# Kernel optimization log

Hardware: AMD Instinct MI355X
Metric: run time of the kernel (lower is better)

Reference implementation:

```python
import jax, jax.numpy as jnp
import numpy as np

N, E, G, F = 100000, 3200000, 256, 15
NEG_SLOPE = 0.2


def _lin(k, fi, fo):
    s = 1.0 / np.sqrt(fi)
    return jax.random.uniform(k, (fi, fo), jnp.float32, -s, s)


def _vec(k, n, fi):
    s = 1.0 / np.sqrt(fi)
    return jax.random.uniform(k, (n,), jnp.float32, -s, s)


def setup_inputs() -> dict:
    key = jax.random.key(0)
    ks = jax.random.split(key, 40)
    inp = {}
    inp["x"] = jax.random.normal(ks[0], (N, F), jnp.float32)
    inp["edge_index"] = jax.random.randint(ks[1], (2, E), 0, N, dtype=jnp.int32)
    inp["batch"] = jnp.sort(jax.random.randint(ks[2], (N,), 0, G, dtype=jnp.int32))
    inp["xA"] = jax.random.normal(ks[3], (G, 300), jnp.float32)
    i = 4
    for l in (1, 2, 3):
        inp[f"cW{l}"] = _lin(ks[i], F, F); i += 1
        inp[f"cas{l}"] = _vec(ks[i], F, F); i += 1
        inp[f"cad{l}"] = _vec(ks[i], F, F); i += 1
        inp[f"cb{l}"] = jnp.zeros((F,), jnp.float32)
        inp[f"fW{l}"] = _lin(ks[i], F, F); i += 1
        inp[f"fb{l}"] = _vec(ks[i], F, F); i += 1
    inp["m1W"] = _lin(ks[i], 90, 90); i += 1
    inp["m1b"] = _vec(ks[i], 90, 90); i += 1
    inp["aW1"] = _lin(ks[i], 300, 300); i += 1
    inp["ab1"] = _vec(ks[i], 300, 300); i += 1
    inp["aW2"] = _lin(ks[i], 300, 300); i += 1
    inp["ab2"] = _vec(ks[i], 300, 300); i += 1
    inp["aW3"] = _lin(ks[i], 300, 300); i += 1
    inp["ab3"] = _vec(ks[i], 300, 300); i += 1
    inp["aW4"] = _lin(ks[i], 300, 45); i += 1
    inp["ab4"] = _vec(ks[i], 45, 300); i += 1
    inp["m2W"] = _lin(ks[i], 90, 1); i += 1
    inp["m2b"] = _vec(ks[i], 1, 90); i += 1
    return inp


def _gat(x, src, dst, W, a_s, a_d, b):
    """PyG GATConv (heads=1, add_self_loops handled by caller via src/dst)."""
    h = x @ W                                        # [N, F]
    e = jax.nn.leaky_relu((h @ a_s)[src] + (h @ a_d)[dst], NEG_SLOPE)  # [E+N]
    mx = jax.ops.segment_max(e, dst, num_segments=N)
    ex = jnp.exp(e - mx[dst])
    den = jax.ops.segment_sum(ex, dst, num_segments=N)
    alpha = ex / (den[dst] + 1e-16)                   # segment softmax over dst
    out = jax.ops.segment_sum(h[src] * alpha[:, None], dst, num_segments=N)
    return out + b


def reference(x, edge_index, batch, xA,
              cW1, cas1, cad1, cb1, fW1, fb1,
              cW2, cas2, cad2, cb2, fW2, fb2,
              cW3, cas3, cad3, cb3, fW3, fb3,
              m1W, m1b, aW1, ab1, aW2, ab2, aW3, ab3, aW4, ab4,
              m2W, m2b):
    loop = jnp.arange(N, dtype=edge_index.dtype)      # self loops
    src = jnp.concatenate([edge_index[0], loop])
    dst = jnp.concatenate([edge_index[1], loop])

    h = _gat(x, src, dst, cW1, cas1, cad1, cb1)
    h = jax.nn.relu(h @ fW1 + fb1)
    h = _gat(h, src, dst, cW2, cas2, cad2, cb2)
    h = jax.nn.relu(h @ fW2 + fb2)
    h = _gat(h, src, dst, cW3, cas3, cad3, cb3)
    h = h @ fW3 + fb3

    s = jax.ops.segment_sum(h, batch, num_segments=G)
    mx = jax.ops.segment_max(h, batch, num_segments=G)
    cnt = jax.ops.segment_sum(jnp.ones((N, 1), h.dtype), batch, num_segments=G)
    mean = s / jnp.maximum(cnt, 1.0)
    pooled = jnp.concatenate([s, mx, mean], axis=1)   # [G, 45]

    a = jax.nn.relu(xA @ aW1 + ab1)
    a = jax.nn.relu(a @ aW2 + ab2)
    a = jax.nn.sigmoid(a @ aW3 + ab3)
    xann = a @ aW4 + ab4                              # [G, 45]

    z = jnp.concatenate([pooled, xann], axis=1)       # [G, 90]
    z = jax.nn.relu(z @ m1W + m1b)
    z = z @ m2W + m2b
    return jax.nn.sigmoid(z)
```

## Files before the change

kernel.cpp:

```cpp
#include <hip/hip_runtime.h>
#include <hip/hip_bf16.h>
#include <math.h>

#define FDIM 15
#define FPAD 16
#define NEG_SLOPE 0.2f
#define BSH 8
#define BWID 256
#define HB_GRID 256
#define HB_BLK 1024

typedef _Float16 half_t;

__device__ __forceinline__ float leaky(float e) {
  return fmaxf(NEG_SLOPE * e, e);
}

__global__ void k_zero(int* __restrict__ p, int n) {
  int i = blockIdx.x * blockDim.x + threadIdx.x;
  if (i < n) p[i] = 0;
}

__global__ void k_bhist(const int* __restrict__ dstI, int* __restrict__ bcnt,
                        int n_tot, int n_real, int NB) {
  __shared__ int hist[512];
  int tid = threadIdx.x;
  for (int i = tid; i < NB; i += blockDim.x) hist[i] = 0;
  __syncthreads();
  int stride = gridDim.x * blockDim.x;
  for (int i = blockIdx.x * blockDim.x + tid; i < n_tot; i += stride) {
    int d = (i < n_real) ? dstI[i] : (i - n_real);
    atomicAdd(&hist[d >> BSH], 1);
  }
  __syncthreads();
  for (int i = tid; i < NB; i += blockDim.x)
    if (hist[i]) atomicAdd(&bcnt[i], hist[i]);
}

__global__ void k_bscan(const int* __restrict__ bcnt, int* __restrict__ boff,
                        int* __restrict__ bcur, int* __restrict__ rowptr,
                        int NB, int N, int total) {
  __shared__ int s[512];
  int tid = threadIdx.x;
  int v = (tid < NB) ? bcnt[tid] : 0;
  s[tid] = v;
  __syncthreads();
  for (int off = 1; off < 512; off <<= 1) {
    int add = (tid >= off) ? s[tid - off] : 0;
    __syncthreads();
    s[tid] += add;
    __syncthreads();
  }
  if (tid < NB) { int e = s[tid] - v; boff[tid] = e; bcur[tid] = e; }
  if (tid == NB - 1) boff[NB] = s[tid];
  if (tid == 0) rowptr[N] = total;
}

__global__ void k_bpart(const int* __restrict__ srcI, const int* __restrict__ dstI,
                        int* __restrict__ bcur, int* __restrict__ bbuf,
                        int n_tot, int n_real, int NB) {
  __shared__ int hist[512];
  __shared__ int base[512];
  int tid = threadIdx.x;
  for (int i = tid; i < NB; i += blockDim.x) hist[i] = 0;
  __syncthreads();
  int stride = gridDim.x * blockDim.x;
  int g0 = blockIdx.x * blockDim.x + tid;
  for (int i = g0; i < n_tot; i += stride) {
    int d = (i < n_real) ? dstI[i] : (i - n_real);
    atomicAdd(&hist[d >> BSH], 1);
  }
  __syncthreads();
  for (int i = tid; i < NB; i += blockDim.x)
    base[i] = hist[i] ? atomicAdd(&bcur[i], hist[i]) : 0;
  __syncthreads();
  for (int i = tid; i < NB; i += blockDim.x) hist[i] = 0;
  __syncthreads();
  for (int i = g0; i < n_tot; i += stride) {
    int s, d;
    if (i < n_real) { s = srcI[i]; d = dstI[i]; }
    else { s = d = i - n_real; }
    int b = d >> BSH;
    int p = base[b] + atomicAdd(&hist[b], 1);
    bbuf[p] = (s << BSH) | (d & (BWID - 1));
  }
}

__global__ void k_bbuild(const int* __restrict__ boff, const int* __restrict__ bbuf,
                         int* __restrict__ rowptr, int* __restrict__ csr, int N) {
  __shared__ int hist[BWID];
  __shared__ int sc[BWID];
  int b = blockIdx.x;
  int tid = threadIdx.x;
  int base_dst = b << BSH;
  int nd = min(BWID, N - base_dst);
  int s0 = boff[b], s1 = boff[b + 1];
  if (tid < BWID) hist[tid] = 0;
  __syncthreads();
  for (int j = s0 + tid; j < s1; j += 512)
    atomicAdd(&hist[bbuf[j] & (BWID - 1)], 1);
  __syncthreads();
  int v = 0;
  if (tid < BWID) { v = hist[tid]; sc[tid] = v; }
  __syncthreads();
  for (int off = 1; off < BWID; off <<= 1) {
    int add = 0;
    if (tid < BWID && tid >= off) add = sc[tid - off];
    __syncthreads();
    if (tid < BWID) sc[tid] += add;
    __syncthreads();
  }
  if (tid < nd) rowptr[base_dst + tid] = s0 + sc[tid] - v;
  __syncthreads();
  if (tid < BWID) hist[tid] = sc[tid] - v;
  __syncthreads();
  for (int j = s0 + tid; j < s1; j += 512) {
    int e = bbuf[j];
    int dl = e & (BWID - 1);
    int p = s0 + atomicAdd(&hist[dl], 1);
    csr[p] = (e >> BSH) << 5;
  }
}

__global__ void k_transform(const float* __restrict__ in, int ld_in,
                            const float* __restrict__ W,
                            const float* __restrict__ a_s,
                            const float* __restrict__ a_d,
                            half_t* __restrict__ hp,
                            float* __restrict__ ad_,
                            int n_nodes) {
  __shared__ float Ws[FDIM * FDIM];
  __shared__ float asv[FDIM], adv[FDIM];
  int tid = threadIdx.x;
  if (tid < FDIM * FDIM) Ws[tid] = W[tid];
  if (tid < FDIM) { asv[tid] = a_s[tid]; adv[tid] = a_d[tid]; }
  __syncthreads();
  int n = blockIdx.x * blockDim.x + tid;
  if (n >= n_nodes) return;
  float xin[FDIM];
#pragma unroll
  for (int j = 0; j < FDIM; ++j) xin[j] = in[n * ld_in + j];
  float sa = 0.f, da = 0.f;
  half_t hrow[FPAD];
#pragma unroll
  for (int o = 0; o < FDIM; ++o) {
    float acc = 0.f;
#pragma unroll
    for (int k = 0; k < FDIM; ++k) acc += xin[k] * Ws[k * FDIM + o];
    hrow[o] = (half_t)acc;
    sa += acc * asv[o];
    da += acc * adv[o];
  }
  hrow[FDIM] = (half_t)sa;
  ad_[n] = da;
  float4 w0, w1;
  __builtin_memcpy(&w0, &hrow[0], 16);
  __builtin_memcpy(&w1, &hrow[8], 16);
  float4* dst = (float4*)(hp + (size_t)n * FPAD);
  dst[0] = w0;
  dst[1] = w1;
}

__global__ void k_gat(const int* __restrict__ rowptr, const int* __restrict__ csrB,
                      const half_t* __restrict__ hp, const float* __restrict__ ad_,
                      const float* __restrict__ cb, const float* __restrict__ fW,
                      const float* __restrict__ fb,
                      const float* __restrict__ nW, const float* __restrict__ nas,
                      const float* __restrict__ nad,
                      half_t* __restrict__ hp2, float* __restrict__ ad2,
                      float* __restrict__ fout,
                      int n_nodes, int do_relu, int fuse) {
  __shared__ float Ws[FDIM * FDIM];
  __shared__ float W2s[FDIM * FDIM];
  __shared__ float cbv[FDIM], fbv[FDIM], as2v[FDIM], ad2v[FDIM];
  __shared__ float aggT[16][16];
  __shared__ float outT[16][16];
  int tid = threadIdx.x;
  if (tid < FDIM * FDIM) Ws[tid] = fW[tid];
  if (tid < FDIM) { cbv[tid] = cb[tid]; fbv[tid] = fb[tid]; }
  if (fuse) {
    if (tid < FDIM * FDIM) W2s[tid] = nW[tid];
    if (tid < FDIM) { as2v[tid] = nas[tid]; ad2v[tid] = nad[tid]; }
  }
  __syncthreads();
  int dl = tid >> 4;
  int f  = tid & 15;
  int d  = blockIdx.x * 16 + dl;
  float val = 0.f;
  if (d < n_nodes) {
    int rs = rowptr[d], re = rowptr[d + 1];
    float adv = ad_[d];
    const char* hb = (const char*)hp;
    int fo = f << 1;
    float den0 = 0.f, acc0 = 0.f, den1 = 0.f, acc1 = 0.f;
    int j = rs;
    for (; j + 7 < re; j += 8) {
      int o0 = csrB[j],     o1 = csrB[j + 1], o2 = csrB[j + 2], o3 = csrB[j + 3];
      int o4 = csrB[j + 4], o5 = csrB[j + 5], o6 = csrB[j + 6], o7 = csrB[j + 7];
      float hv0 = (float)*(const half_t*)(hb + o0 + fo);
      float hv1 = (float)*(const half_t*)(hb + o1 + fo);
      float hv2 = (float)*(const half_t*)(hb + o2 + fo);
      float hv3 = (float)*(const half_t*)(hb + o3 + fo);
      float hv4 = (float)*(const half_t*)(hb + o4 + fo);
      float hv5 = (float)*(const half_t*)(hb + o5 + fo);
      float hv6 = (float)*(const half_t*)(hb + o6 + fo);
      float hv7 = (float)*(const half_t*)(hb + o7 + fo);
      float w0 = __expf(leaky(__shfl(hv0, 15, 16) + adv));
      float w1 = __expf(leaky(__shfl(hv1, 15, 16) + adv));
      float w2 = __expf(leaky(__shfl(hv2, 15, 16) + adv));
      float w3 = __expf(leaky(__shfl(hv3, 15, 16) + adv));
      float w4 = __expf(leaky(__shfl(hv4, 15, 16) + adv));
      float w5 = __expf(leaky(__shfl(hv5, 15, 16) + adv));
      float w6 = __expf(leaky(__shfl(hv6, 15, 16) + adv));
      float w7 = __expf(leaky(__shfl(hv7, 15, 16) + adv));
      den0 += w0; acc0 += hv0 * w0;
      den1 += w1; acc1 += hv1 * w1;
      den0 += w2; acc0 += hv2 * w2;
      den1 += w3; acc1 += hv3 * w3;
      den0 += w4; acc0 += hv4 * w4;
      den1 += w5; acc1 += hv5 * w5;
      den0 += w6; acc0 += hv6 * w6;
      den1 += w7; acc1 += hv7 * w7;
    }
    for (; j < re; ++j) {
      int o0 = csrB[j];
      float hv0 = (float)*(const half_t*)(hb + o0 + fo);
      float w0 = __expf(leaky(__shfl(hv0, 15, 16) + adv));
      den0 += w0; acc0 += hv0 * w0;
    }
    val = (acc0 + acc1) / (den0 + den1 + 1e-16f);
  }
  aggT[dl][f] = (f < FDIM) ? (val + cbv[f]) : 0.f;
  __syncthreads();
  int o = f;
  float ffn = 0.f;
  if (o < FDIM) {
    ffn = fbv[o];
#pragma unroll
    for (int k = 0; k < FDIM; ++k) ffn += aggT[dl][k] * Ws[k * FDIM + o];
    if (do_relu) ffn = fmaxf(ffn, 0.f);
  }
  if (!fuse) {
    if (d < n_nodes) fout[d * FPAD + o] = (o < FDIM) ? ffn : 0.f;
    return;
  }
  outT[dl][o] = ffn;
  __syncthreads();
  if (d < n_nodes) {
    float h2 = 0.f;
    if (o < FDIM) {
#pragma unroll
      for (int k = 0; k < FDIM; ++k) h2 += outT[dl][k] * W2s[k * FDIM + o];
    }
    float pa = (o < FDIM) ? h2 * as2v[o] : 0.f;
    float pd = (o < FDIM) ? h2 * ad2v[o] : 0.f;
#pragma unroll
    for (int k = 8; k; k >>= 1) {
      pa += __shfl_xor(pa, k, 16);
      pd += __shfl_xor(pd, k, 16);
    }
    hp2[(size_t)d * FPAD + o] = (half_t)((o < FDIM) ? h2 : pa);
    if (o == 0) ad2[d] = pd;
  }
}

__device__ __forceinline__ int lowerb(const int* __restrict__ a, int n, int key) {
  int lo = 0, hi = n;
  while (lo < hi) { int mid = (lo + hi) >> 1; if (a[mid] < key) lo = mid + 1; else hi = mid; }
  return lo;
}

__global__ void k_pool(const float* __restrict__ fout, const int* __restrict__ batch,
                       float* __restrict__ pooled, int n_nodes) {
  __shared__ float ss[256], sm[256];
  int g = blockIdx.x;
  int tid = threadIdx.x;
  int s = lowerb(batch, n_nodes, g);
  int e = lowerb(batch, n_nodes, g + 1);
  int f = tid & 15;
  float sum = 0.f, mx = -INFINITY;
  for (int n = s + (tid >> 4); n < e; n += 16) {
    float v = fout[n * FPAD + f];
    sum += v;
    mx = fmaxf(mx, v);
  }
  ss[tid] = sum; sm[tid] = mx;
  __syncthreads();
  for (int step = 128; step >= 16; step >>= 1) {
    if (tid < step) { ss[tid] += ss[tid + step]; sm[tid] = fmaxf(sm[tid], sm[tid + step]); }
    __syncthreads();
  }
  if (tid < FDIM) {
    float cnt = (float)(e - s);
    float sv = ss[tid];
    pooled[g * 45 + tid] = sv;
    pooled[g * 45 + 15 + tid] = sm[tid];
    pooled[g * 45 + 30 + tid] = sv / fmaxf(cnt, 1.f);
  }
}

__global__ void k_ann(const float* __restrict__ xA,
                      const float* __restrict__ aW1, const float* __restrict__ ab1,
                      const float* __restrict__ aW2, const float* __restrict__ ab2,
                      const float* __restrict__ aW3, const float* __restrict__ ab3,
                      const float* __restrict__ aW4, const float* __restrict__ ab4,
                      const float* __restrict__ m1W, const float* __restrict__ m1b,
                      const float* __restrict__ m2W, const float* __restrict__ m2b,
                      const float* __restrict__ pooled,
                      float* __restrict__ out) {
  __shared__ float za[304], zb[304];
  int g = blockIdx.x;
  int t = threadIdx.x;
  for (int k = t; k < 300; k += 320) za[k] = xA[g * 300 + k];
  __syncthreads();
  if (t < 300) {
    float acc = ab1[t];
#pragma unroll 10
    for (int k = 0; k < 300; ++k) acc += za[k] * aW1[k * 300 + t];
    zb[t] = fmaxf(acc, 0.f);
  }
  __syncthreads();
  if (t < 300) {
    float acc = ab2[t];
#pragma unroll 10
    for (int k = 0; k < 300; ++k) acc += zb[k] * aW2[k * 300 + t];
    za[t] = fmaxf(acc, 0.f);
  }
  __syncthreads();
  if (t < 300) {
    float acc = ab3[t];
#pragma unroll 10
    for (int k = 0; k < 300; ++k) acc += za[k] * aW3[k * 300 + t];
    zb[t] = 1.f / (1.f + expf(-acc));
  }
  __syncthreads();
  if (t < 45) {
    float acc = ab4[t];
#pragma unroll 10
    for (int k = 0; k < 300; ++k) acc += zb[k] * aW4[k * 45 + t];
    za[45 + t] = acc;
  } else if (t < 90) {
    za[t - 45] = pooled[g * 45 + (t - 45)];
  }
  __syncthreads();
  if (t < 90) {
    float acc = m1b[t];
#pragma unroll 10
    for (int k = 0; k < 90; ++k) acc += za[k] * m1W[k * 90 + t];
    zb[t] = fmaxf(acc, 0.f);
  }
  __syncthreads();
  if (t == 0) {
    float acc = m2b[0];
#pragma unroll 10
    for (int k = 0; k < 90; ++k) acc += zb[k] * m2W[k];
    out[g] = 1.f / (1.f + expf(-acc));
  }
}

extern "C" void kernel_launch(void* const* d_in, const int* in_sizes, int n_in,
                              void* d_out, int out_size, void* d_ws, size_t ws_size,
                              hipStream_t stream) {
  const float* x   = (const float*)d_in[0];
  const int* ei    = (const int*)d_in[1];
  const int* batch = (const int*)d_in[2];
  const float* xA  = (const float*)d_in[3];

  const int N = in_sizes[0] / FDIM;
  const int E = in_sizes[1] / 2;
  const int G = in_sizes[3] / 300;
  const int ET = E + N;
  const int NB = (N + BWID - 1) >> BSH;

  const int* srcI = ei;
  const int* dstI = ei + E;

  float* ws = (float*)d_ws;
  size_t layerW = (size_t)34 * N;
  size_t uSize = layerW > (size_t)ET ? layerW : (size_t)ET;
  size_t off = 0;
  int*    bbuf = (int*)(ws + off);
  half_t* hpA  = (half_t*)(ws + off);
  half_t* hpB  = (half_t*)(ws + off + (size_t)8 * N);
  float*  adA  = ws + off + (size_t)16 * N;
  float*  adB  = ws + off + (size_t)17 * N;
  float*  fout = ws + off + (size_t)18 * N;
  off += uSize;
  int*   rowptr = (int*)(ws + off); off += N + 1;
  int*   csr    = (int*)(ws + off); off += (size_t)ET;
  int*   bcnt   = (int*)(ws + off); off += 516;
  int*   boff   = (int*)(ws + off); off += 516;
  int*   bcur   = (int*)(ws + off); off += 516;
  float* pooled = ws + off; off += (size_t)G * 45;

  const int B = 256;
  const int gN = (N + B - 1) / B;

  k_zero<<<(NB + B - 1) / B, B, 0, stream>>>(bcnt, NB);
  k_bhist<<<HB_GRID, HB_BLK, 0, stream>>>(dstI, bcnt, ET, E, NB);
  k_bscan<<<1, 512, 0, stream>>>(bcnt, boff, bcur, rowptr, NB, N, ET);
  k_bpart<<<HB_GRID, HB_BLK, 0, stream>>>(srcI, dstI, bcur, bbuf, ET, E, NB);
  k_bbuild<<<NB, 512, 0, stream>>>(boff, bbuf, rowptr, csr, N);

  const float* cW1  = (const float*)d_in[4];
  const float* cas1 = (const float*)d_in[5];
  const float* cad1 = (const float*)d_in[6];
  const float* cb1  = (const float*)d_in[7];
  const float* fW1  = (const float*)d_in[8];
  const float* fb1  = (const float*)d_in[9];
  const float* cW2  = (const float*)d_in[10];
  const float* cas2 = (const float*)d_in[11];
  const float* cad2 = (const float*)d_in[12];
  const float* cb2  = (const float*)d_in[13];
  const float* fW2  = (const float*)d_in[14];
  const float* fb2  = (const float*)d_in[15];
  const float* cW3  = (const float*)d_in[16];
  const float* cas3 = (const float*)d_in[17];
  const float* cad3 = (const float*)d_in[18];
  const float* cb3  = (const float*)d_in[19];
  const float* fW3  = (const float*)d_in[20];
  const float* fb3  = (const float*)d_in[21];

  const int gGat = (N + 15) / 16;
  k_transform<<<gN, B, 0, stream>>>(x, FDIM, cW1, cas1, cad1, hpA, adA, N);
  k_gat<<<gGat, B, 0, stream>>>(rowptr, csr, hpA, adA, cb1, fW1, fb1,
                                cW2, cas2, cad2, hpB, adB, nullptr, N, 1, 1);
  k_gat<<<gGat, B, 0, stream>>>(rowptr, csr, hpB, adB, cb2, fW2, fb2,
                                cW3, cas3, cad3, hpA, adA, nullptr, N, 1, 1);
  k_gat<<<gGat, B, 0, stream>>>(rowptr, csr, hpA, adA, cb3, fW3, fb3,
                                nullptr, nullptr, nullptr, nullptr, nullptr, fout,
                                N, 0, 0);

  k_pool<<<G, B, 0, stream>>>(fout, batch, pooled, N);

  const float* m1W = (const float*)d_in[22];
  const float* m1b = (const float*)d_in[23];
  const float* aW1 = (const float*)d_in[24];
  const float* ab1 = (const float*)d_in[25];
  const float* aW2 = (const float*)d_in[26];
  const float* ab2 = (const float*)d_in[27];
  const float* aW3 = (const float*)d_in[28];
  const float* ab3 = (const float*)d_in[29];
  const float* aW4 = (const float*)d_in[30];
  const float* ab4 = (const float*)d_in[31];
  const float* m2W = (const float*)d_in[32];
  const float* m2b = (const float*)d_in[33];

  k_ann<<<G, 320, 0, stream>>>(xA, aW1, ab1, aW2, ab2, aW3, ab3, aW4, ab4,
                               m1W, m1b, m2W, m2b, pooled, (float*)d_out);
}
```

Baseline: 395.7 us.

## Batch eight graphs per block in ANN MLP kernel to reuse weight loads

The ANN/MLP head kernel now processes eight graphs per block instead of one. Each weight element loaded from global memory is reused across all eight activation rows, and activations are read as float4 from shared memory. This cuts redundant weight traffic from 256 blocks down to 32, at the cost of fewer blocks (less parallelism) and more registers per thread.

Result: slower. 463.0 us (+17.0%).

```diff
diff --git a/kernel.cpp b/kernel.cpp
--- a/kernel.cpp
+++ b/kernel.cpp
@@ -9,6 +9,7 @@
 #define BWID 256
 #define HB_GRID 256
 #define HB_BLK 1024
+#define ANN_GPB 8
 
 typedef _Float16 half_t;
 
@@ -299,62 +300,100 @@
   }
 }
 
-__global__ void k_ann(const float* __restrict__ xA,
-                      const float* __restrict__ aW1, const float* __restrict__ ab1,
-                      const float* __restrict__ aW2, const float* __restrict__ ab2,
-                      const float* __restrict__ aW3, const float* __restrict__ ab3,
-                      const float* __restrict__ aW4, const float* __restrict__ ab4,
-                      const float* __restrict__ m1W, const float* __restrict__ m1b,
-                      const float* __restrict__ m2W, const float* __restrict__ m2b,
-                      const float* __restrict__ pooled,
-                      float* __restrict__ out) {
-  __shared__ float za[304], zb[304];
-  int g = blockIdx.x;
+__global__ void __launch_bounds__(512) k_ann(
+    const float* __restrict__ xA,
+    const float* __restrict__ aW1, const float* __restrict__ ab1,
+    const float* __restrict__ aW2, const float* __restrict__ ab2,
+    const float* __restrict__ aW3, const float* __restrict__ ab3,
+    const float* __restrict__ aW4, const float* __restrict__ ab4,
+    const float* __restrict__ m1W, const float* __restrict__ m1b,
+    const float* __restrict__ m2W, const float* __restrict__ m2b,
+    const float* __restrict__ pooled,
+    float* __restrict__ out, int Gt) {
+  __shared__ float bufA[ANN_GPB][304];
+  __shared__ float bufB[ANN_GPB][304];
+  __shared__ float z2[ANN_GPB][90];
+  __shared__ float m2s[90];
+  int g0 = blockIdx.x * ANN_GPB;
   int t = threadIdx.x;
-  for (int k = t; k < 300; k += 320) za[k] = xA[g * 300 + k];
-  __syncthreads();
-  if (t < 300) {
-    float acc = ab1[t];
-#pragma unroll 10
-    for (int k = 0; k < 300; ++k) acc += za[k] * aW1[k * 300 + t];
-    zb[t] = fmaxf(acc, 0.f);
-  }
-  __syncthreads();
-  if (t < 300) {
-    float acc = ab2[t];
-#pragma unroll 10
-    for (int k = 0; k < 300; ++k) acc += zb[k] * aW2[k * 300 + t];
-    za[t] = fmaxf(acc, 0.f);
-  }
-  __syncthreads();
-  if (t < 300) {
-    float acc = ab3[t];
-#pragma unroll 10
-    for (int k = 0; k < 300; ++k) acc += za[k] * aW3[k * 300 + t];
-    zb[t] = 1.f / (1.f + expf(-acc));
-  }
-  __syncthreads();
+  for (int i = t; i < ANN_GPB * 300; i += 512) {
+    int g = i / 300, k = i - g * 300;
+    int gr = g0 + g;
+    bufA[g][k] = (gr < Gt) ? xA[(size_t)gr * 300 + k] : 0.f;
+  }
+  if (t < 90) m2s[t] = m2W[t];
+  __syncthreads();
+  float (*ins)[304] = bufA;
+  float (*outs)[304] = bufB;
+  const float* Ws_[3] = {aW1, aW2, aW3};
+  const float* bs_[3] = {ab1, ab2, ab3};
+  for (int s = 0; s < 3; ++s) {
+    const float* __restrict__ W = Ws_[s];
+    if (t < 300) {
+      float acc[ANN_GPB];
+      float b = bs_[s][t];
+#pragma unroll
+      for (int g = 0; g < ANN_GPB; ++g) acc[g] = b;
+      for (int k = 0; k < 300; k += 4) {
+        float w0 = W[k * 300 + t];
+        float w1 = W[(k + 1) * 300 + t];
+        float w2 = W[(k + 2) * 300 + t];
+        float w3 = W[(k + 3) * 300 + t];
+#pragma unroll
+        for (int g = 0; g < ANN_GPB; ++g) {
+          float4 a = *(const float4*)&ins[g][k];
+          acc[g] += a.x * w0 + a.y * w1 + a.z * w2 + a.w * w3;
+        }
+      }
+#pragma unroll
+      for (int g = 0; g < ANN_GPB; ++g) {
+        float v = acc[g];
+        outs[g][t] = (s < 2) ? fmaxf(v, 0.f) : 1.f / (1.f + expf(-v));
+      }
+    }
+    __syncthreads();
+    float (*tmp)[304] = ins; ins = outs; outs = tmp;
+  }
   if (t < 45) {
-    float acc = ab4[t];
-#pragma unroll 10
-    for (int k = 0; k < 300; ++k) acc += zb[k] * aW4[k * 45 + t];
-    za[45 + t] = acc;
-  } else if (t < 90) {
-    za[t - 45] = pooled[g * 45 + (t - 45)];
-  }
-  __syncthreads();
-  if (t < 90) {
-    float acc = m1b[t];
-#pragma unroll 10
-    for (int k = 0; k < 90; ++k) acc += za[k] * m1W[k * 90 + t];
-    zb[t] = fmaxf(acc, 0.f);
-  }
-  __syncthreads();
-  if (t == 0) {
+    float acc[ANN_GPB];
+    float b = ab4[t];
+#pragma unroll
+    for (int g = 0; g < ANN_GPB; ++g) acc[g] = b;
+    for (int k = 0; k < 300; k += 4) {
+      float w0 = aW4[k * 45 + t];
+      float w1 = aW4[(k + 1) * 45 + t];
+      float w2 = aW4[(k + 2) * 45 + t];
+      float w3 = aW4[(k + 3) * 45 + t];
+#pragma unroll
+      for (int g = 0; g < ANN_GPB; ++g) {
+        float4 a = *(const float4*)&ins[g][k];
+        acc[g] += a.x * w0 + a.y * w1 + a.z * w2 + a.w * w3;
+      }
+    }
+#pragma unroll
+    for (int g = 0; g < ANN_GPB; ++g) outs[g][45 + t] = acc[g];
+  }
+  for (int i = t; i < ANN_GPB * 45; i += 512) {
+    int g = i / 45, j = i - g * 45;
+    int gr = g0 + g;
+    outs[g][j] = (gr < Gt) ? pooled[(size_t)gr * 45 + j] : 0.f;
+  }
+  __syncthreads();
+  for (int i = t; i < ANN_GPB * 90; i += 512) {
+    int g = i / 90, j = i - g * 90;
+    float acc = m1b[j];
+    for (int k = 0; k < 90; k += 2) {
+      float w0 = m1W[k * 90 + j];
+      float w1 = m1W[(k + 1) * 90 + j];
+      acc += outs[g][k] * w0 + outs[g][k + 1] * w1;
+    }
+    z2[g][j] = fmaxf(acc, 0.f);
+  }
+  __syncthreads();
+  if (t < ANN_GPB && g0 + t < Gt) {
     float acc = m2b[0];
-#pragma unroll 10
-    for (int k = 0; k < 90; ++k) acc += zb[k] * m2W[k];
-    out[g] = 1.f / (1.f + expf(-acc));
+    for (int k = 0; k < 90; ++k) acc += z2[t][k] * m2s[k];
+    out[g0 + t] = 1.f / (1.f + expf(-acc));
   }
 }
 
@@ -446,6 +485,7 @@
   const float* m2W = (const float*)d_in[32];
   const float* m2b = (const float*)d_in[33];
 
-  k_ann<<<G, 320, 0, stream>>>(xA, aW1, ab1, aW2, ab2, aW3, ab3, aW4, ab4,
-                               m1W, m1b, m2W, m2b, pooled, (float*)d_out);
-}
+  k_ann<<<(G + ANN_GPB - 1) / ANN_GPB, 512, 0, stream>>>(
+      xA, aW1, ab1, aW2, ab2, aW3, ab3, aW4, ab4,
+      m1W, m1b, m2W, m2b, pooled, (float*)d_out, G);
+}
```
